# Optimization experiments

Hardware: AMD Instinct MI355X
Metric: run time of the kernel (lower is better)

## Reference

```python
import jax, jax.numpy as jnp
import numpy as np

HS_ENC, HS_DEC, ATTN = 1024, 1024, 1024
N, T = 32, 2048


def setup_inputs() -> dict:
    key = jax.random.key(0)
    k1, k2, k3, k4, k5, k6 = jax.random.split(key, 6)
    h_dec = jax.random.normal(k1, (N, HS_DEC), dtype=jnp.float32)
    h_enc = jax.random.normal(k2, (N, T, HS_ENC), dtype=jnp.float32)
    src_lens = jax.random.randint(k3, (N,), 1, T + 1, dtype=jnp.int32)
    # params of nn.Linear(hs_enc+hs_dec, attn_size) and score vector v
    W = jax.random.normal(k4, (ATTN, HS_DEC + HS_ENC), dtype=jnp.float32) * 0.02
    b = jax.random.normal(k5, (ATTN,), dtype=jnp.float32) * 0.02
    v = jax.random.normal(k6, (ATTN,), dtype=jnp.float32)
    return {"h_dec": h_dec, "h_enc": h_enc, "src_lens": src_lens, "W": W, "b": b, "v": v}


def reference(h_dec, h_enc, src_lens, W, b, v):
    # Linear over concat(h_dec, h_enc) == sum of split projections; avoids
    # materializing the repeated/concatenated [N, T, hs_dec+hs_enc] tensor.
    hs_dec = h_dec.shape[-1]
    Wd, We = W[:, :hs_dec], W[:, hs_dec:]          # [A, hs_dec], [A, hs_enc]
    dec_proj = jnp.einsum('nd,ad->na', h_dec, Wd)  # [N, A]
    enc_proj = jnp.einsum('nte,ae->nta', h_enc, We)  # [N, T, A]
    attn_out = jnp.tanh(dec_proj[:, None, :] + enc_proj + b)  # [N, T, A]
    score = jnp.einsum('nta,a->nt', attn_out, v)   # [N, T]
    T_ = h_enc.shape[1]
    mask = jnp.arange(T_)[None, :] < src_lens[:, None]
    score = jnp.where(mask, score, jnp.float32(-1e10))
    weights = jax.nn.softmax(score, axis=-1)       # [N, T]
    ctx = jnp.einsum('nt,nte->ne', weights, h_enc) # [N, hs_enc]
    return ctx, weights
```

## Files before the change

kernel.cpp:

```cpp
#include <hip/hip_runtime.h>
#include <hip/hip_fp16.h>

#define HS 1024
#define TT 2048

typedef _Float16 half8 __attribute__((ext_vector_type(8)));
typedef float floatx4 __attribute__((ext_vector_type(4)));

__device__ __forceinline__ void dma16(const _Float16* g, _Float16* l) {
    __builtin_amdgcn_global_load_lds(
        (const __attribute__((address_space(1))) unsigned int*)g,
        (__attribute__((address_space(3))) unsigned int*)l, 16, 0, 0);
}

__global__ __launch_bounds__(256) void k_dproj(const float* __restrict__ h_dec,
                                               const float* __restrict__ W,
                                               const float* __restrict__ bias,
                                               float* __restrict__ dproj) {
    int wid = blockIdx.x * 4 + (threadIdx.x >> 6);
    int lane = threadIdx.x & 63;
    int n = wid >> 10, a = wid & 1023;
    const float4* hd = reinterpret_cast<const float4*>(h_dec + (size_t)n * HS);
    const float4* wr = reinterpret_cast<const float4*>(W + (size_t)a * 2048);
    float s = 0.f;
#pragma unroll
    for (int i = 0; i < 4; ++i) {
        float4 h = hd[lane + i * 64];
        float4 w = wr[lane + i * 64];
        s += h.x * w.x + h.y * w.y + h.z * w.z + h.w * w.w;
    }
    for (int off = 32; off; off >>= 1) s += __shfl_xor(s, off);
    if (lane == 0) dproj[wid] = bias[a] + s;
}

__global__ __launch_bounds__(256) void k_cvtW(const float* __restrict__ W,
                                              _Float16* __restrict__ We16) {
    int idx4 = (blockIdx.x * 256 + threadIdx.x) * 4;
    int a = idx4 >> 10;
    int e = idx4 & 1023;
    float4 f = *reinterpret_cast<const float4*>(W + (size_t)a * 2048 + 1024 + e);
    _Float16 h0 = (_Float16)f.x, h1 = (_Float16)f.y, h2 = (_Float16)f.z, h3 = (_Float16)f.w;
    ushort4 p;
    p.x = *(unsigned short*)&h0; p.y = *(unsigned short*)&h1;
    p.z = *(unsigned short*)&h2; p.w = *(unsigned short*)&h3;
    *reinterpret_cast<ushort4*>(We16 + idx4) = p;
}

__global__ __launch_bounds__(256) void k_cvtA(const float* __restrict__ h_enc,
                                              _Float16* __restrict__ h_enc16) {
    size_t idx = ((size_t)blockIdx.x * 256 + threadIdx.x) * 16;
    const float4* g = reinterpret_cast<const float4*>(h_enc + idx);
    _Float16 h[16];
#pragma unroll
    for (int i = 0; i < 4; ++i) {
        float4 f = g[i];
        h[i * 4 + 0] = (_Float16)f.x; h[i * 4 + 1] = (_Float16)f.y;
        h[i * 4 + 2] = (_Float16)f.z; h[i * 4 + 3] = (_Float16)f.w;
    }
    *reinterpret_cast<uint4*>(h_enc16 + idx)     = *reinterpret_cast<uint4*>(&h[0]);
    *reinterpret_cast<uint4*>(h_enc16 + idx + 8) = *reinterpret_cast<uint4*>(&h[8]);
}

__global__ __launch_bounds__(512, 2) void k_score8(
        const _Float16* __restrict__ h_enc16, const _Float16* __restrict__ We16,
        const float* __restrict__ dproj, const float* __restrict__ v,
        float* __restrict__ scores) {
    __shared__ _Float16 As[4][256 * 32];
    __shared__ _Float16 Bs[4][256 * 32];
    __shared__ float s_acc[256];

    const int tid = threadIdx.x;
    const int ord = ((blockIdx.x & 7) << 7) | (blockIdx.x >> 3);
    const int aT = ord & 3, tT = (ord >> 2) & 7, n = ord >> 5;
    const int t0 = tT << 8, a0 = aT << 8;

    if (tid < 256) s_acc[tid] = 0.0f;

    const int w = tid >> 6, lane = tid & 63;
    const int wm = w >> 2, wn = w & 3;
    const int col = lane & 15, quad = lane >> 4;

    const _Float16* srcA[2];
    const _Float16* srcB[2];
#pragma unroll
    for (int c = 0; c < 2; ++c) {
        int Gp = c * 512 + tid;
        int Gl = Gp ^ ((Gp >> 3) & 7);
        int r = Gl >> 2, g = Gl & 3;
        srcA[c] = h_enc16 + ((size_t)(n * TT + t0 + r)) * HS + g * 8;
        srcB[c] = We16 + ((size_t)(a0 + r)) * HS + g * 8;
    }

    int offA[8], offB[4];
#pragma unroll
    for (int mi = 0; mi < 8; ++mi) {
        int r = wm * 128 + mi * 16 + col;
        offA[mi] = (r * 64 + quad * 16) ^ (((r >> 1) & 7) << 4);
    }
#pragma unroll
    for (int ni = 0; ni < 4; ++ni) {
        int r = wn * 64 + ni * 16 + col;
        offB[ni] = (r * 64 + quad * 16) ^ (((r >> 1) & 7) << 4);
    }

    floatx4 acc[8][4];
#pragma unroll
    for (int mi = 0; mi < 8; ++mi)
#pragma unroll
        for (int ni = 0; ni < 4; ++ni) acc[mi][ni] = (floatx4)0.0f;

    auto issue2 = [&](int kt, int c) {
        const int b = kt & 3;
        dma16(srcA[c] + kt * 32, &As[b][c * 4096 + w * 512]);
        dma16(srcB[c] + kt * 32, &Bs[b][c * 4096 + w * 512]);
    };

#pragma unroll
    for (int kt = 0; kt < 3; ++kt) { issue2(kt, 0); issue2(kt, 1); }

    for (int kt = 0; kt < 32; ++kt) {
        const int b = kt & 3;
        if (kt < 30)       asm volatile("s_waitcnt vmcnt(8)" ::: "memory");
        else if (kt == 30) asm volatile("s_waitcnt vmcnt(4)" ::: "memory");
        else               asm volatile("s_waitcnt vmcnt(0)" ::: "memory");
        __builtin_amdgcn_s_barrier();
        __builtin_amdgcn_sched_barrier(0);

        const char* Ab = (const char*)As[b];
        const char* Bb = (const char*)Bs[b];
        half8 af[4], bf[4];
#pragma unroll
        for (int ni = 0; ni < 4; ++ni)
            bf[ni] = *reinterpret_cast<const half8*>(Bb + offB[ni]);
#pragma unroll
        for (int mi = 0; mi < 4; ++mi)
            af[mi] = *reinterpret_cast<const half8*>(Ab + offA[mi]);
        if (kt < 29) issue2(kt + 3, 0);
        __builtin_amdgcn_s_setprio(1);
#pragma unroll
        for (int mi = 0; mi < 4; ++mi)
#pragma unroll
            for (int ni = 0; ni < 4; ++ni)
                acc[mi][ni] = __builtin_amdgcn_mfma_f32_16x16x32_f16(
                    af[mi], bf[ni], acc[mi][ni], 0, 0, 0);
        __builtin_amdgcn_s_setprio(0);

#pragma unroll
        for (int mi = 0; mi < 4; ++mi)
            af[mi] = *reinterpret_cast<const half8*>(Ab + offA[4 + mi]);
        if (kt < 29) issue2(kt + 3, 1);
        __builtin_amdgcn_s_setprio(1);
#pragma unroll
        for (int mi = 0; mi < 4; ++mi)
#pragma unroll
            for (int ni = 0; ni < 4; ++ni)
                acc[4 + mi][ni] = __builtin_amdgcn_mfma_f32_16x16x32_f16(
                    af[mi], bf[ni], acc[4 + mi][ni], 0, 0, 0);
        __builtin_amdgcn_s_setprio(0);
    }

    float vv[4], dd[4];
#pragma unroll
    for (int ni = 0; ni < 4; ++ni) {
        const int a = a0 + wn * 64 + ni * 16 + col;
        vv[ni] = v[a];
        dd[ni] = dproj[n * HS + a];
    }
#pragma unroll
    for (int mi = 0; mi < 8; ++mi) {
#pragma unroll
        for (int rg = 0; rg < 4; ++rg) {
            float s = 0.0f;
#pragma unroll
            for (int ni = 0; ni < 4; ++ni) {
                float x = acc[mi][ni][rg] + dd[ni];
                float e2 = __expf(2.0f * x);
                float th = 1.0f - 2.0f * __builtin_amdgcn_rcpf(e2 + 1.0f);
                s += vv[ni] * th;
            }
            s += __shfl_xor(s, 8);
            s += __shfl_xor(s, 4);
            s += __shfl_xor(s, 2);
            s += __shfl_xor(s, 1);
            if (col == 0)
                atomicAdd(&s_acc[wm * 128 + mi * 16 + quad * 4 + rg], s);
        }
    }
    __syncthreads();
    if (tid < 256)
        atomicAdd(&scores[(size_t)n * TT + t0 + tid], s_acc[tid]);
}

__global__ __launch_bounds__(256) void k_softmax(float* __restrict__ wout,
                                                 const int* __restrict__ lens) {
    __shared__ float red[4];
    __shared__ float red2[4];
    int n = blockIdx.x, tid = threadIdx.x;
    int len = lens[n];
    float* row = wout + (size_t)n * TT;
    float sv[8];
    float m = -3.0e38f;
#pragma unroll
    for (int i = 0; i < 8; ++i) {
        int t = tid + i * 256;
        float s = row[t];
        s = (t < len) ? s : -1.0e10f;
        sv[i] = s;
        m = fmaxf(m, s);
    }
    for (int off = 1; off <= 32; off <<= 1) m = fmaxf(m, __shfl_xor(m, off));
    if ((tid & 63) == 0) red[tid >> 6] = m;
    __syncthreads();
    m = fmaxf(fmaxf(red[0], red[1]), fmaxf(red[2], red[3]));
    float sum = 0.f, es[8];
#pragma unroll
    for (int i = 0; i < 8; ++i) { es[i] = __expf(sv[i] - m); sum += es[i]; }
    for (int off = 1; off <= 32; off <<= 1) sum += __shfl_xor(sum, off);
    if ((tid & 63) == 0) red2[tid >> 6] = sum;
    __syncthreads();
    sum = red2[0] + red2[1] + red2[2] + red2[3];
    float rinv = 1.0f / sum;
#pragma unroll
    for (int i = 0; i < 8; ++i) row[tid + i * 256] = es[i] * rinv;
}

__global__ __launch_bounds__(256) void k_ctx(const _Float16* __restrict__ h_enc16,
                                             const float* __restrict__ wts,
                                             float* __restrict__ ctx) {
    __shared__ float red[256][8];
    int b = blockIdx.x;
    int n  = b >> 4;
    int ec = (b >> 2) & 3;
    int ts = b & 3;
    int tid = threadIdx.x;
    int q = tid & 31, tg = tid >> 5;
    int e = ec * 256 + q * 8;
    float acc[8];
#pragma unroll
    for (int j = 0; j < 8; ++j) acc[j] = 0.f;
    const float* wrow = wts + (size_t)n * TT;
    for (int t = ts * 512 + tg; t < ts * 512 + 512; t += 8) {
        float w = wrow[t];
        uint4 raw = *reinterpret_cast<const uint4*>(
            h_enc16 + ((size_t)(n * TT + t)) * HS + e);
        const _Float16* hp = reinterpret_cast<const _Float16*>(&raw);
#pragma unroll
        for (int j = 0; j < 8; ++j) acc[j] += w * (float)hp[j];
    }
#pragma unroll
    for (int j = 0; j < 8; ++j) red[tid][j] = acc[j];
    __syncthreads();
    if (tid < 32) {
        float s[8];
#pragma unroll
        for (int j = 0; j < 8; ++j) s[j] = red[tid][j];
        for (int g = 1; g < 8; ++g)
#pragma unroll
            for (int j = 0; j < 8; ++j) s[j] += red[g * 32 + tid][j];
        float* dst = ctx + (size_t)n * HS + ec * 256 + tid * 8;
#pragma unroll
        for (int j = 0; j < 8; ++j) atomicAdd(dst + j, s[j]);
    }
}

__global__ __launch_bounds__(256) void k_score_naive(const float* __restrict__ h_enc,
                                                     const float* __restrict__ W,
                                                     const float* __restrict__ dproj,
                                                     const float* __restrict__ v,
                                                     float* __restrict__ scores) {
    int gw = blockIdx.x * 4 + (threadIdx.x >> 6);
    int lane = threadIdx.x & 63;
    int n = gw >> 11, t = gw & 2047;
    const float4* he = reinterpret_cast<const float4*>(h_enc + ((size_t)(n * TT + t)) * HS);
    float4 hv[4];
#pragma unroll
    for (int i = 0; i < 4; ++i) hv[i] = he[lane + i * 64];
    float s = 0.f;
    for (int a = 0; a < 1024; ++a) {
        const float4* wr = reinterpret_cast<const float4*>(W + (size_t)a * 2048 + 1024);
        float d = 0.f;
#pragma unroll
        for (int i = 0; i < 4; ++i) {
            float4 wv = wr[lane + i * 64];
            d += hv[i].x * wv.x + hv[i].y * wv.y + hv[i].z * wv.z + hv[i].w * wv.w;
        }
        for (int off = 32; off; off >>= 1) d += __shfl_xor(d, off);
        s += v[a] * tanhf(d + dproj[n * HS + a]);
    }
    if (lane == 0) scores[(size_t)n * TT + t] = s;
}

__global__ __launch_bounds__(256) void k_ctx_naive(const float* __restrict__ h_enc,
                                                   const float* __restrict__ wts,
                                                   float* __restrict__ ctx) {
    int n = blockIdx.x;
    int e = threadIdx.x * 4;
    float4 a = make_float4(0.f, 0.f, 0.f, 0.f);
    const float* wrow = wts + (size_t)n * TT;
    for (int t = 0; t < TT; ++t) {
        float w = wrow[t];
        float4 h = *reinterpret_cast<const float4*>(h_enc + ((size_t)(n * TT + t)) * HS + e);
        a.x += w * h.x; a.y += w * h.y; a.z += w * h.z; a.w += w * h.w;
    }
    *reinterpret_cast<float4*>(ctx + (size_t)n * HS + e) = a;
}

extern "C" void kernel_launch(void* const* d_in, const int* in_sizes, int n_in,
                              void* d_out, int out_size, void* d_ws, size_t ws_size,
                              hipStream_t stream) {
    const float* h_dec    = (const float*)d_in[0];
    const float* h_enc    = (const float*)d_in[1];
    const int*   src_lens = (const int*)d_in[2];
    const float* W = (const float*)d_in[3];
    const float* b = (const float*)d_in[4];
    const float* v = (const float*)d_in[5];

    float* out = (float*)d_out;
    float* ctx = out;
    float* wts = out + 32 * 1024;

    float*    dproj   = (float*)d_ws;
    _Float16* We16    = (_Float16*)((char*)d_ws + 131072);
    _Float16* h_enc16 = (_Float16*)((char*)d_ws + 131072 + 2097152);
    const size_t need = 131072 + 2097152 + (size_t)32 * TT * HS * 2;

    k_dproj<<<8192, 256, 0, stream>>>(h_dec, W, b, dproj);
    if (ws_size >= need) {
        (void)hipMemsetAsync(ctx, 0, 32 * 1024 * sizeof(float), stream);
        (void)hipMemsetAsync(wts, 0, (size_t)32 * TT * sizeof(float), stream);
        k_cvtW <<<1024, 256, 0, stream>>>(W, We16);
        k_cvtA <<<16384, 256, 0, stream>>>(h_enc, h_enc16);
        k_score8<<<1024, 512, 0, stream>>>(h_enc16, We16, dproj, v, wts);
        k_softmax<<<32, 256, 0, stream>>>(wts, src_lens);
        k_ctx  <<<512, 256, 0, stream>>>(h_enc16, wts, ctx);
    } else {
        k_score_naive<<<16384, 256, 0, stream>>>(h_enc, W, dproj, v, wts);
        k_softmax<<<32, 256, 0, stream>>>(wts, src_lens);
        k_ctx_naive<<<32, 256, 0, stream>>>(h_enc, wts, ctx);
    }
}
```

Baseline: 599.7 us.

## Restructure GEMM main loop with split A/B DMA issue and extra barriers

```diff
diff --git a/kernel.cpp b/kernel.cpp
--- a/kernel.cpp
+++ b/kernel.cpp
@@ -109,33 +109,41 @@
 #pragma unroll
         for (int ni = 0; ni < 4; ++ni) acc[mi][ni] = (floatx4)0.0f;
 
-    auto issue2 = [&](int kt, int c) {
+    auto issueA = [&](int kt) {
         const int b = kt & 3;
-        dma16(srcA[c] + kt * 32, &As[b][c * 4096 + w * 512]);
-        dma16(srcB[c] + kt * 32, &Bs[b][c * 4096 + w * 512]);
+#pragma unroll
+        for (int c = 0; c < 2; ++c)
+            dma16(srcA[c] + kt * 32, &As[b][c * 4096 + w * 512]);
     };
-
-#pragma unroll
-    for (int kt = 0; kt < 3; ++kt) { issue2(kt, 0); issue2(kt, 1); }
-
-    for (int kt = 0; kt < 32; ++kt) {
+    auto issueB = [&](int kt) {
         const int b = kt & 3;
-        if (kt < 30)       asm volatile("s_waitcnt vmcnt(8)" ::: "memory");
-        else if (kt == 30) asm volatile("s_waitcnt vmcnt(4)" ::: "memory");
-        else               asm volatile("s_waitcnt vmcnt(0)" ::: "memory");
-        __builtin_amdgcn_s_barrier();
-        __builtin_amdgcn_sched_barrier(0);
-
+#pragma unroll
+        for (int c = 0; c < 2; ++c)
+            dma16(srcB[c] + kt * 32, &Bs[b][c * 4096 + w * 512]);
+    };
+
+#pragma unroll
+    for (int kt = 0; kt < 3; ++kt) { issueA(kt); issueB(kt); }
+    asm volatile("s_waitcnt vmcnt(8)" ::: "memory");
+    __builtin_amdgcn_s_barrier();
+
+    for (int j = 0; j < 32; ++j) {
+        const int b = j & 3;
         const char* Ab = (const char*)As[b];
         const char* Bb = (const char*)Bs[b];
         half8 af[4], bf[4];
+
 #pragma unroll
         for (int ni = 0; ni < 4; ++ni)
             bf[ni] = *reinterpret_cast<const half8*>(Bb + offB[ni]);
 #pragma unroll
         for (int mi = 0; mi < 4; ++mi)
             af[mi] = *reinterpret_cast<const half8*>(Ab + offA[mi]);
-        if (kt < 29) issue2(kt + 3, 0);
+        if (j < 29) issueA(j + 3);
+        __builtin_amdgcn_sched_barrier(0);
+        __builtin_amdgcn_s_barrier();
+        asm volatile("s_waitcnt lgkmcnt(0)" ::: "memory");
+        __builtin_amdgcn_sched_barrier(0);
         __builtin_amdgcn_s_setprio(1);
 #pragma unroll
         for (int mi = 0; mi < 4; ++mi)
@@ -144,11 +152,17 @@
                 acc[mi][ni] = __builtin_amdgcn_mfma_f32_16x16x32_f16(
                     af[mi], bf[ni], acc[mi][ni], 0, 0, 0);
         __builtin_amdgcn_s_setprio(0);
+        __builtin_amdgcn_sched_barrier(0);
+        __builtin_amdgcn_s_barrier();
 
 #pragma unroll
         for (int mi = 0; mi < 4; ++mi)
             af[mi] = *reinterpret_cast<const half8*>(Ab + offA[4 + mi]);
-        if (kt < 29) issue2(kt + 3, 1);
+        if (j < 29) issueB(j + 3);
+        __builtin_amdgcn_sched_barrier(0);
+        __builtin_amdgcn_s_barrier();
+        asm volatile("s_waitcnt lgkmcnt(0)" ::: "memory");
+        __builtin_amdgcn_sched_barrier(0);
         __builtin_amdgcn_s_setprio(1);
 #pragma unroll
         for (int mi = 0; mi < 4; ++mi)
@@ -157,6 +171,11 @@
                 acc[4 + mi][ni] = __builtin_amdgcn_mfma_f32_16x16x32_f16(
                     af[mi], bf[ni], acc[4 + mi][ni], 0, 0, 0);
         __builtin_amdgcn_s_setprio(0);
+        if (j < 29)       asm volatile("s_waitcnt vmcnt(8)" ::: "memory");
+        else if (j == 29) asm volatile("s_waitcnt vmcnt(4)" ::: "memory");
+        else if (j == 30) asm volatile("s_waitcnt vmcnt(0)" ::: "memory");
+        __builtin_amdgcn_sched_barrier(0);
+        __builtin_amdgcn_s_barrier();
     }
 
     float vv[4], dd[4];
```

New measurement: 598.3 us. No clear change (-0.2%).

## Fuse preprocessing kernels, skip masked tiles, and merge softmax with context

Applied to the files above, without the earlier changes.

```diff
diff --git a/kernel.cpp b/kernel.cpp
--- a/kernel.cpp
+++ b/kernel.cpp
@@ -13,58 +13,72 @@
         (__attribute__((address_space(3))) unsigned int*)l, 16, 0, 0);
 }
 
-__global__ __launch_bounds__(256) void k_dproj(const float* __restrict__ h_dec,
-                                               const float* __restrict__ W,
-                                               const float* __restrict__ bias,
-                                               float* __restrict__ dproj) {
-    int wid = blockIdx.x * 4 + (threadIdx.x >> 6);
-    int lane = threadIdx.x & 63;
-    int n = wid >> 10, a = wid & 1023;
-    const float4* hd = reinterpret_cast<const float4*>(h_dec + (size_t)n * HS);
-    const float4* wr = reinterpret_cast<const float4*>(W + (size_t)a * 2048);
-    float s = 0.f;
-#pragma unroll
-    for (int i = 0; i < 4; ++i) {
-        float4 h = hd[lane + i * 64];
-        float4 w = wr[lane + i * 64];
-        s += h.x * w.x + h.y * w.y + h.z * w.z + h.w * w.w;
-    }
-    for (int off = 32; off; off >>= 1) s += __shfl_xor(s, off);
-    if (lane == 0) dproj[wid] = bias[a] + s;
-}
-
-__global__ __launch_bounds__(256) void k_cvtW(const float* __restrict__ W,
-                                              _Float16* __restrict__ We16) {
-    int idx4 = (blockIdx.x * 256 + threadIdx.x) * 4;
-    int a = idx4 >> 10;
-    int e = idx4 & 1023;
-    float4 f = *reinterpret_cast<const float4*>(W + (size_t)a * 2048 + 1024 + e);
-    _Float16 h0 = (_Float16)f.x, h1 = (_Float16)f.y, h2 = (_Float16)f.z, h3 = (_Float16)f.w;
-    ushort4 p;
-    p.x = *(unsigned short*)&h0; p.y = *(unsigned short*)&h1;
-    p.z = *(unsigned short*)&h2; p.w = *(unsigned short*)&h3;
-    *reinterpret_cast<ushort4*>(We16 + idx4) = p;
-}
-
-__global__ __launch_bounds__(256) void k_cvtA(const float* __restrict__ h_enc,
-                                              _Float16* __restrict__ h_enc16) {
-    size_t idx = ((size_t)blockIdx.x * 256 + threadIdx.x) * 16;
-    const float4* g = reinterpret_cast<const float4*>(h_enc + idx);
-    _Float16 h[16];
-#pragma unroll
-    for (int i = 0; i < 4; ++i) {
-        float4 f = g[i];
-        h[i * 4 + 0] = (_Float16)f.x; h[i * 4 + 1] = (_Float16)f.y;
-        h[i * 4 + 2] = (_Float16)f.z; h[i * 4 + 3] = (_Float16)f.w;
-    }
-    *reinterpret_cast<uint4*>(h_enc16 + idx)     = *reinterpret_cast<uint4*>(&h[0]);
-    *reinterpret_cast<uint4*>(h_enc16 + idx + 8) = *reinterpret_cast<uint4*>(&h[8]);
+__global__ __launch_bounds__(256) void k_pre(const float* __restrict__ h_enc,
+                                             _Float16* __restrict__ h_enc16,
+                                             const float* __restrict__ h_dec,
+                                             const float* __restrict__ W,
+                                             const float* __restrict__ bias,
+                                             const int* __restrict__ lens,
+                                             float* __restrict__ dproj,
+                                             _Float16* __restrict__ We16,
+                                             float* __restrict__ sc,
+                                             float* __restrict__ ctx) {
+    const int b = blockIdx.x;
+    const int tid = threadIdx.x;
+    if (b < 16384) {
+        const int n = b >> 9;
+        const int t4 = (b & 511) * 4;
+        const int lim = (lens[n] + 255) & ~255;
+        if (t4 >= lim) return;
+        size_t idx = ((size_t)b * 256 + tid) * 16;
+        const float4* g = reinterpret_cast<const float4*>(h_enc + idx);
+        _Float16 h[16];
+#pragma unroll
+        for (int i = 0; i < 4; ++i) {
+            float4 f = g[i];
+            h[i * 4 + 0] = (_Float16)f.x; h[i * 4 + 1] = (_Float16)f.y;
+            h[i * 4 + 2] = (_Float16)f.z; h[i * 4 + 3] = (_Float16)f.w;
+        }
+        *reinterpret_cast<uint4*>(h_enc16 + idx)     = *reinterpret_cast<uint4*>(&h[0]);
+        *reinterpret_cast<uint4*>(h_enc16 + idx + 8) = *reinterpret_cast<uint4*>(&h[8]);
+    } else if (b < 24576) {
+        int wid = (b - 16384) * 4 + (tid >> 6);
+        int lane = tid & 63;
+        int n = wid >> 10, a = wid & 1023;
+        const float4* hd = reinterpret_cast<const float4*>(h_dec + (size_t)n * HS);
+        const float4* wr = reinterpret_cast<const float4*>(W + (size_t)a * 2048);
+        float s = 0.f;
+#pragma unroll
+        for (int i = 0; i < 4; ++i) {
+            float4 h = hd[lane + i * 64];
+            float4 w = wr[lane + i * 64];
+            s += h.x * w.x + h.y * w.y + h.z * w.z + h.w * w.w;
+        }
+        for (int off = 32; off; off >>= 1) s += __shfl_xor(s, off);
+        if (lane == 0) dproj[wid] = bias[a] + s;
+    } else if (b < 25600) {
+        int idx4 = ((b - 24576) * 256 + tid) * 4;
+        int a = idx4 >> 10;
+        int e = idx4 & 1023;
+        float4 f = *reinterpret_cast<const float4*>(W + (size_t)a * 2048 + 1024 + e);
+        _Float16 h0 = (_Float16)f.x, h1 = (_Float16)f.y, h2 = (_Float16)f.z, h3 = (_Float16)f.w;
+        ushort4 p;
+        p.x = *(unsigned short*)&h0; p.y = *(unsigned short*)&h1;
+        p.z = *(unsigned short*)&h2; p.w = *(unsigned short*)&h3;
+        *reinterpret_cast<ushort4*>(We16 + idx4) = p;
+    } else if (b < 25664) {
+        reinterpret_cast<float4*>(sc)[(b - 25600) * 256 + tid] =
+            make_float4(0.f, 0.f, 0.f, 0.f);
+    } else {
+        reinterpret_cast<float4*>(ctx)[(b - 25664) * 256 + tid] =
+            make_float4(0.f, 0.f, 0.f, 0.f);
+    }
 }
 
 __global__ __launch_bounds__(512, 2) void k_score8(
         const _Float16* __restrict__ h_enc16, const _Float16* __restrict__ We16,
         const float* __restrict__ dproj, const float* __restrict__ v,
-        float* __restrict__ scores) {
+        const int* __restrict__ lens, float* __restrict__ scores) {
     __shared__ _Float16 As[4][256 * 32];
     __shared__ _Float16 Bs[4][256 * 32];
     __shared__ float s_acc[256];
@@ -73,6 +87,8 @@
     const int ord = ((blockIdx.x & 7) << 7) | (blockIdx.x >> 3);
     const int aT = ord & 3, tT = (ord >> 2) & 7, n = ord >> 5;
     const int t0 = tT << 8, a0 = aT << 8;
+
+    if (t0 >= lens[n]) return;
 
     if (tid < 256) s_acc[tid] = 0.0f;
 
@@ -191,6 +207,132 @@
         atomicAdd(&scores[(size_t)n * TT + t0 + tid], s_acc[tid]);
 }
 
+__global__ __launch_bounds__(256) void k_ctxsm(const _Float16* __restrict__ h_enc16,
+                                               const float* __restrict__ sc,
+                                               const int* __restrict__ lens,
+                                               float* __restrict__ wts,
+                                               float* __restrict__ ctx) {
+    __shared__ float red[4], red2[4];
+    __shared__ float racc[256][8];
+    const int b = blockIdx.x;
+    const int n = b >> 4, ec = (b >> 2) & 3, ts = b & 3;
+    const int tid = threadIdx.x;
+    const int len = lens[n];
+    const float* srow = sc + (size_t)n * TT;
+
+    float sv[8];
+    float m = -3.0e38f;
+#pragma unroll
+    for (int i = 0; i < 8; ++i) {
+        int t = tid + i * 256;
+        float s = srow[t];
+        s = (t < len) ? s : -1.0e10f;
+        sv[i] = s;
+        m = fmaxf(m, s);
+    }
+    for (int off = 1; off <= 32; off <<= 1) m = fmaxf(m, __shfl_xor(m, off));
+    if ((tid & 63) == 0) red[tid >> 6] = m;
+    __syncthreads();
+    m = fmaxf(fmaxf(red[0], red[1]), fmaxf(red[2], red[3]));
+    float sum = 0.f;
+#pragma unroll
+    for (int i = 0; i < 8; ++i) sum += __expf(sv[i] - m);
+    for (int off = 1; off <= 32; off <<= 1) sum += __shfl_xor(sum, off);
+    if ((tid & 63) == 0) red2[tid >> 6] = sum;
+    __syncthreads();
+    sum = red2[0] + red2[1] + red2[2] + red2[3];
+    const float rinv = 1.0f / sum;
+
+    if (ec == 0) {
+#pragma unroll
+        for (int j = 0; j < 2; ++j) {
+            int t = ts * 512 + j * 256 + tid;
+            float s = srow[t];
+            s = (t < len) ? s : -1.0e10f;
+            wts[(size_t)n * TT + t] = __expf(s - m) * rinv;
+        }
+    }
+
+    if (ts * 512 < len) {
+        const int tend = min(ts * 512 + 512, len);
+        const int q = tid & 31, tg = tid >> 5;
+        const int e = ec * 256 + q * 8;
+        float acc[8];
+#pragma unroll
+        for (int j = 0; j < 8; ++j) acc[j] = 0.f;
+        for (int t = ts * 512 + tg; t < tend; t += 8) {
+            float w = __expf(srow[t] - m) * rinv;
+            uint4 raw = *reinterpret_cast<const uint4*>(
+                h_enc16 + ((size_t)(n * TT + t)) * HS + e);
+            const _Float16* hp = reinterpret_cast<const _Float16*>(&raw);
+#pragma unroll
+            for (int j = 0; j < 8; ++j) acc[j] += w * (float)hp[j];
+        }
+#pragma unroll
+        for (int j = 0; j < 8; ++j) racc[tid][j] = acc[j];
+        __syncthreads();
+        if (tid < 32) {
+            float s2[8];
+#pragma unroll
+            for (int j = 0; j < 8; ++j) s2[j] = racc[tid][j];
+            for (int g = 1; g < 8; ++g)
+#pragma unroll
+                for (int j = 0; j < 8; ++j) s2[j] += racc[g * 32 + tid][j];
+            float* dst = ctx + (size_t)n * HS + ec * 256 + tid * 8;
+#pragma unroll
+            for (int j = 0; j < 8; ++j) atomicAdd(dst + j, s2[j]);
+        }
+    }
+}
+
+__global__ __launch_bounds__(256) void k_dproj(const float* __restrict__ h_dec,
+                                               const float* __restrict__ W,
+                                               const float* __restrict__ bias,
+                                               float* __restrict__ dproj) {
+    int wid = blockIdx.x * 4 + (threadIdx.x >> 6);
+    int lane = threadIdx.x & 63;
+    int n = wid >> 10, a = wid & 1023;
+    const float4* hd = reinterpret_cast<const float4*>(h_dec + (size_t)n * HS);
+    const float4* wr = reinterpret_cast<const float4*>(W + (size_t)a * 2048);
+    float s = 0.f;
+#pragma unroll
+    for (int i = 0; i < 4; ++i) {
+        float4 h = hd[lane + i * 64];
+        float4 w = wr[lane + i * 64];
+        s += h.x * w.x + h.y * w.y + h.z * w.z + h.w * w.w;
+    }
+    for (int off = 32; off; off >>= 1) s += __shfl_xor(s, off);
+    if (lane == 0) dproj[wid] = bias[a] + s;
+}
+
+__global__ __launch_bounds__(256) void k_cvtW(const float* __restrict__ W,
+                                              _Float16* __restrict__ We16) {
+    int idx4 = (blockIdx.x * 256 + threadIdx.x) * 4;
+    int a = idx4 >> 10;
+    int e = idx4 & 1023;
+    float4 f = *reinterpret_cast<const float4*>(W + (size_t)a * 2048 + 1024 + e);
+    _Float16 h0 = (_Float16)f.x, h1 = (_Float16)f.y, h2 = (_Float16)f.z, h3 = (_Float16)f.w;
+    ushort4 p;
+    p.x = *(unsigned short*)&h0; p.y = *(unsigned short*)&h1;
+    p.z = *(unsigned short*)&h2; p.w = *(unsigned short*)&h3;
+    *reinterpret_cast<ushort4*>(We16 + idx4) = p;
+}
+
+__global__ __launch_bounds__(256) void k_cvtA(const float* __restrict__ h_enc,
+                                              _Float16* __restrict__ h_enc16) {
+    size_t idx = ((size_t)blockIdx.x * 256 + threadIdx.x) * 16;
+    const float4* g = reinterpret_cast<const float4*>(h_enc + idx);
+    _Float16 h[16];
+#pragma unroll
+    for (int i = 0; i < 4; ++i) {
+        float4 f = g[i];
+        h[i * 4 + 0] = (_Float16)f.x; h[i * 4 + 1] = (_Float16)f.y;
+        h[i * 4 + 2] = (_Float16)f.z; h[i * 4 + 3] = (_Float16)f.w;
+    }
+    *reinterpret_cast<uint4*>(h_enc16 + idx)     = *reinterpret_cast<uint4*>(&h[0]);
+    *reinterpret_cast<uint4*>(h_enc16 + idx + 8) = *reinterpret_cast<uint4*>(&h[8]);
+}
+
 __global__ __launch_bounds__(256) void k_softmax(float* __restrict__ wout,
                                                  const int* __restrict__ lens) {
     __shared__ float red[4];
@@ -322,18 +464,27 @@
     float*    dproj   = (float*)d_ws;
     _Float16* We16    = (_Float16*)((char*)d_ws + 131072);
     _Float16* h_enc16 = (_Float16*)((char*)d_ws + 131072 + 2097152);
-    const size_t need = 131072 + 2097152 + (size_t)32 * TT * HS * 2;
-
-    k_dproj<<<8192, 256, 0, stream>>>(h_dec, W, b, dproj);
-    if (ws_size >= need) {
+    float*    sc      = (float*)((char*)d_ws + 131072 + 2097152 +
+                                 (size_t)32 * TT * HS * 2);
+    const size_t need_mid = 131072 + 2097152 + (size_t)32 * TT * HS * 2;
+    const size_t need_new = need_mid + (size_t)32 * TT * sizeof(float);
+
+    if (ws_size >= need_new) {
+        k_pre   <<<25696, 256, 0, stream>>>(h_enc, h_enc16, h_dec, W, b, src_lens,
+                                            dproj, We16, sc, ctx);
+        k_score8<<<1024, 512, 0, stream>>>(h_enc16, We16, dproj, v, src_lens, sc);
+        k_ctxsm <<<512, 256, 0, stream>>>(h_enc16, sc, src_lens, wts, ctx);
+    } else if (ws_size >= need_mid) {
+        k_dproj<<<8192, 256, 0, stream>>>(h_dec, W, b, dproj);
         (void)hipMemsetAsync(ctx, 0, 32 * 1024 * sizeof(float), stream);
         (void)hipMemsetAsync(wts, 0, (size_t)32 * TT * sizeof(float), stream);
         k_cvtW <<<1024, 256, 0, stream>>>(W, We16);
         k_cvtA <<<16384, 256, 0, stream>>>(h_enc, h_enc16);
-        k_score8<<<1024, 512, 0, stream>>>(h_enc16, We16, dproj, v, wts);
+        k_score8<<<1024, 512, 0, stream>>>(h_enc16, We16, dproj, v, src_lens, wts);
         k_softmax<<<32, 256, 0, stream>>>(wts, src_lens);
         k_ctx  <<<512, 256, 0, stream>>>(h_enc16, wts, ctx);
     } else {
+        k_dproj<<<8192, 256, 0, stream>>>(h_dec, W, b, dproj);
         k_score_naive<<<16384, 256, 0, stream>>>(h_enc, W, dproj, v, wts);
         k_softmax<<<32, 256, 0, stream>>>(wts, src_lens);
         k_ctx_naive<<<32, 256, 0, stream>>>(h_enc, wts, ctx);
```

Result: faster. 492.5 us (-17.9%).
